# Performance work log

Hardware: AMD Instinct MI355X
Metric: run time of the kernel (lower is better)

Reference implementation:

```python
import jax, jax.numpy as jnp
import numpy as np

TEMPERATURE = 0.1
EPS = 1e-12  # torch F.normalize eps


def _l2_normalize(x):
    n = jnp.linalg.norm(x, axis=1, keepdims=True)
    return x / jnp.maximum(n, EPS)


def setup_inputs() -> dict:
    key = jax.random.key(0)
    k1, k2, k3 = jax.random.split(key, 3)
    B, D = 2048, 2048
    return {
        "emb_i": jax.random.normal(k1, (B, D), dtype=jnp.float32),
        "emb_j": jax.random.normal(k2, (B, D), dtype=jnp.float32),
        "emb_k": jax.random.normal(k3, (B, D), dtype=jnp.float32),
    }


def reference(emb_i, emb_j, emb_k):
    Bi, Bj, Bk = emb_i.shape[0], emb_j.shape[0], emb_k.shape[0]
    size = Bi + Bj + Bk
    Bij = Bi + Bj

    z = jnp.concatenate([
        _l2_normalize(emb_i), _l2_normalize(emb_j), _l2_normalize(emb_k)
    ], axis=0)  # [size, D]

    # cosine similarity of normalized rows == dot product
    sim = z @ z.T                      # [size, size]
    e = jnp.exp(sim / TEMPERATURE)     # [size, size]
    diag = jnp.diagonal(e)             # exp(1/T) on the diagonal

    # denominator per row i: sum over all a != i of exp(sim[i,a]/T)
    denom = e.sum(axis=1) - diag       # [size]

    # rows 0..Bij-1: numerator sums over columns 0..Bij-1, excluding j == i
    num1 = e[:Bij, :Bij].sum(axis=1) - diag[:Bij]
    # rows Bij..size-1: numerator sums over columns Bij..size-1, excluding j == i
    num2 = e[Bij:, Bij:].sum(axis=1) - diag[Bij:]

    loss1 = -jnp.log((num1 / (Bij - 1)) / denom[:Bij])
    loss2 = -jnp.log((num2 / (Bk - 1)) / denom[Bij:])
    return (loss1.sum() + loss2.sum()) / size
```

## Files before the change

kernel.cpp:

```cpp
#include <hip/hip_runtime.h>
#include <hip/hip_bf16.h>

#define SIZE 6144
#define DDIM 2048
#define BHALF 2048
#define BIJ 4096
#define NT 48

typedef __attribute__((ext_vector_type(4))) float f32x4;
typedef __attribute__((ext_vector_type(4))) int i32x4;
typedef __attribute__((ext_vector_type(8))) int i32x8;

__device__ __forceinline__ float block_reduce_sum(float v, float* red) {
    #pragma unroll
    for (int off = 32; off; off >>= 1) v += __shfl_xor(v, off, 64);
    int lane = threadIdx.x & 63, wid = threadIdx.x >> 6;
    if (lane == 0) red[wid] = v;
    __syncthreads();
    float t = red[0] + red[1] + red[2] + red[3];
    __syncthreads();
    return t;
}

__global__ __launch_bounds__(256) void normalize_kernel(
    const float* __restrict__ ei, const float* __restrict__ ej,
    const float* __restrict__ ek,
    unsigned char* __restrict__ zb4, float* __restrict__ dii,
    float* __restrict__ S)
{
    __shared__ float red[4];
    int r = blockIdx.x;
    if (r < 48) S[r * 256 + threadIdx.x] = 0.f;
    const float* src = (r < BHALF)   ? (ei + (size_t)r * DDIM)
                     : (r < 2*BHALF) ? (ej + (size_t)(r - BHALF) * DDIM)
                                     : (ek + (size_t)(r - 2*BHALF) * DDIM);
    int t = threadIdx.x;
    float4 v0 = ((const float4*)src)[t*2];
    float4 v1 = ((const float4*)src)[t*2 + 1];
    float ss = v0.x*v0.x + v0.y*v0.y + v0.z*v0.z + v0.w*v0.w
             + v1.x*v1.x + v1.y*v1.y + v1.z*v1.z + v1.w*v1.w;
    float tot = block_reduce_sum(ss, red);
    float scale = 64.0f / fmaxf(sqrtf(tot), 1e-12f);

    float xs[8] = {v0.x, v0.y, v0.z, v0.w, v1.x, v1.y, v1.z, v1.w};
    unsigned int pk = 0;
    float d = 0.f;
    #pragma unroll
    for (int jj = 0; jj < 8; ++jj) {
        float xv = xs[jj] * scale;
        float ax = fabsf(xv);
        unsigned int m = ax < 0.25f ? 0u : ax < 0.75f ? 1u : ax < 1.25f ? 2u
                       : ax < 1.75f ? 3u : ax < 2.5f  ? 4u : ax < 3.5f  ? 5u
                       : ax < 5.0f  ? 6u : 7u;
        float dec    = ax < 0.25f ? 0.f : ax < 0.75f ? 0.5f : ax < 1.25f ? 1.f
                     : ax < 1.75f ? 1.5f : ax < 2.5f ? 2.f : ax < 3.5f ? 3.f
                     : ax < 5.0f  ? 4.f : 6.f;
        d += dec * dec;
        unsigned int c = m | (xv < 0.f ? 8u : 0u);
        pk |= c << (4 * jj);
    }
    ((unsigned int*)zb4)[(size_t)r * 256 + t] = pk;
    float dtot = block_reduce_sum(d, red);
    if (t == 0) dii[r] = dtot * (1.0f / 4096.0f);
}

__global__ __launch_bounds__(256) void simexp_kernel(
    const unsigned char* __restrict__ zb4, float* __restrict__ S)
{
    __shared__ unsigned char As[2][8192];
    __shared__ unsigned char Bs[2][8192];

    const int x  = blockIdx.x & 7;
    const int j  = blockIdx.x >> 3;
    const int pi = j / 49;
    const int jj = j % 49;
    const int p  = 3 * x + pi;
    int rt, ct;
    if (jj < 48 - p) { rt = p;      ct = p + jj; }
    else             { rt = 47 - p; ct = rt + (jj - (48 - p)); }

    const int tid  = threadIdx.x;
    const int lane = tid & 63;
    const int w    = tid >> 6;
    const int wr   = w >> 1, wc = w & 1;
    const int rowA0 = rt * 128, colB0 = ct * 128;

    const int rowc = lane >> 2;
    const int csw  = (((lane & 3) ^ ((rowc >> 1) & 3))) * 16;

    const int lr = lane & 15;
    const int l4 = lane >> 4;
    const int rsl = ((l4 ^ ((lr >> 1) & 3))) * 16;

    f32x4 acc[4][4] = {};

#define STAGE(buf, kw) do {                                                  \
    _Pragma("unroll")                                                        \
    for (int g2 = 0; g2 < 2; ++g2) {                                         \
        const int g = w * 2 + g2;                                            \
        const unsigned char* ga = zb4                                        \
            + (size_t)(rowA0 + g*16 + rowc) * 1024 + (kw)*64 + csw;          \
        __builtin_amdgcn_global_load_lds(                                    \
            (const __attribute__((address_space(1))) void*)ga,               \
            (__attribute__((address_space(3))) void*)&As[buf][g * 1024],     \
            16, 0, 0);                                                       \
        const unsigned char* gb = zb4                                        \
            + (size_t)(colB0 + g*16 + rowc) * 1024 + (kw)*64 + csw;          \
        __builtin_amdgcn_global_load_lds(                                    \
            (const __attribute__((address_space(1))) void*)gb,               \
            (__attribute__((address_space(3))) void*)&Bs[buf][g * 1024],     \
            16, 0, 0);                                                       \
    }                                                                        \
} while (0)

    STAGE(0, 0);
    __syncthreads();

    for (int t = 0; t < 16; ++t) {
        const int cur = t & 1;
        if (t < 15) STAGE(cur ^ 1, t + 1);

        i32x8 a8[4];
        #pragma unroll
        for (int mi = 0; mi < 4; ++mi) {
            i32x4 tv = *(const i32x4*)&As[cur][(wr*4 + mi)*1024 + lr*64 + rsl];
            a8[mi] = __builtin_shufflevector(tv, tv, 0, 1, 2, 3, -1, -1, -1, -1);
        }
        __builtin_amdgcn_s_setprio(1);
        #pragma unroll
        for (int ni = 0; ni < 4; ++ni) {
            i32x4 tv = *(const i32x4*)&Bs[cur][(wc*4 + ni)*1024 + lr*64 + rsl];
            i32x8 b8 = __builtin_shufflevector(tv, tv, 0, 1, 2, 3, -1, -1, -1, -1);
            #pragma unroll
            for (int mi = 0; mi < 4; ++mi)
                acc[mi][ni] = __builtin_amdgcn_mfma_scale_f32_16x16x128_f8f6f4(
                    a8[mi], b8, acc[mi][ni], 4, 4,
                    0, 0x79797979, 0, 0x79797979);
        }
        __builtin_amdgcn_s_setprio(0);

        if (t < 15) __syncthreads();
    }

    #pragma unroll
    for (int mi = 0; mi < 4; ++mi)
        #pragma unroll
        for (int ni = 0; ni < 4; ++ni)
            #pragma unroll
            for (int q = 0; q < 4; ++q)
                acc[mi][ni][q] = __expf(10.0f * acc[mi][ni][q]);

    {
        float rs[4][4];
        #pragma unroll
        for (int mi = 0; mi < 4; ++mi)
            #pragma unroll
            for (int q = 0; q < 4; ++q) {
                float s = 0.f;
                #pragma unroll
                for (int ni = 0; ni < 4; ++ni) s += acc[mi][ni][q];
                rs[mi][q] = s;
            }
        #pragma unroll
        for (int off = 1; off < 16; off <<= 1)
            #pragma unroll
            for (int mi = 0; mi < 4; ++mi)
                #pragma unroll
                for (int q = 0; q < 4; ++q)
                    rs[mi][q] += __shfl_xor(rs[mi][q], off, 64);

        if ((lane & 15) == 0) {
            float* St = S + ((ct < BIJ / 128) ? 0 : SIZE);
            int rq = l4 * 4;
            #pragma unroll
            for (int mi = 0; mi < 4; ++mi)
                #pragma unroll
                for (int q = 0; q < 4; ++q)
                    atomicAdd(&St[rowA0 + wr*64 + mi*16 + rq + q], rs[mi][q]);
        }
    }

    if (rt != ct) {
        float cs[4];
        #pragma unroll
        for (int ni = 0; ni < 4; ++ni) {
            float s = 0.f;
            #pragma unroll
            for (int mi = 0; mi < 4; ++mi)
                #pragma unroll
                for (int q = 0; q < 4; ++q) s += acc[mi][ni][q];
            cs[ni] = s;
        }
        #pragma unroll
        for (int off = 16; off < 64; off <<= 1)
            #pragma unroll
            for (int ni = 0; ni < 4; ++ni)
                cs[ni] += __shfl_xor(cs[ni], off, 64);

        if (lane < 16) {
            float* St = S + ((rt < BIJ / 128) ? 0 : SIZE);
            #pragma unroll
            for (int ni = 0; ni < 4; ++ni)
                atomicAdd(&St[colB0 + wc*64 + ni*16 + lane], cs[ni]);
        }
    }
}

__global__ __launch_bounds__(256) void loss_kernel(
    const float* __restrict__ S, const float* __restrict__ dii,
    float* __restrict__ out)
{
    __shared__ float red[4];
    float local = 0.f;
    const float c1 = logf((float)(BIJ - 1));
    const float c2 = logf((float)(BHALF - 1));
    for (int r = threadIdx.x; r < SIZE; r += 256) {
        float s1 = S[r], s2 = S[SIZE + r];
        float eii = __expf(10.0f * dii[r]);
        float denom = s1 + s2 - eii;
        float num, c;
        if (r < BIJ) { num = s1 - eii; c = c1; }
        else         { num = s2 - eii; c = c2; }
        local += logf(denom) - logf(num) + c;
    }
    float tot = block_reduce_sum(local, red);
    if (threadIdx.x == 0) out[0] = tot / (float)SIZE;
}

extern "C" void kernel_launch(void* const* d_in, const int* in_sizes, int n_in,
                              void* d_out, int out_size, void* d_ws, size_t ws_size,
                              hipStream_t stream) {
    const float* ei = (const float*)d_in[0];
    const float* ej = (const float*)d_in[1];
    const float* ek = (const float*)d_in[2];
    float* out = (float*)d_out;

    char* ws = (char*)d_ws;
    unsigned char* zb4 = (unsigned char*)ws;
    float* dii = (float*)(ws + 6291456);
    float* S   = (float*)(ws + 6291456 + 24576);

    normalize_kernel<<<dim3(SIZE), dim3(256), 0, stream>>>(ei, ej, ek, zb4, dii, S);
    simexp_kernel<<<dim3(NT * (NT + 1) / 2), dim3(256), 0, stream>>>(zb4, S);
    loss_kernel<<<dim3(1), dim3(256), 0, stream>>>(S, dii, out);
}
```

Before: 78.06 us.

## Split A/B tile staging with fine-grained vmcnt waits and cheaper quantization

The GEMM main loop now issues the A and B tile loads separately, each guarded by its own `s_waitcnt vmcnt` and `s_barrier`. The full `__syncthreads` at the end of each iteration is gone, so the next tile's loads overlap more closely with the current LDS reads and MFMAs. The FP4 e2m1 quantization in the normalize kernel uses a bit-manipulation rounding helper instead of a long chain of compares. The loss kernel merges two logs into one fast `__logf` of the ratio. The hand-written waitcnt assumptions make the schedule fragile, and the fast log and ratio change the rounding slightly.

```diff
diff --git a/kernel.cpp b/kernel.cpp
--- a/kernel.cpp
+++ b/kernel.cpp
@@ -20,6 +20,19 @@
     float t = red[0] + red[1] + red[2] + red[3];
     __syncthreads();
     return t;
+}
+
+__device__ __forceinline__ void quant_e2m1(float xv, unsigned int& code, float& dec) {
+    float ax = fabsf(xv);
+    float y  = fminf(fmaxf(ax, 1.0f), 6.0f);
+    unsigned int u = (__float_as_uint(y) + 0x00200000u) & 0xFFC00000u;
+    float dh = __uint_as_float(u);
+    unsigned int m  = (u >> 22) & 1u;
+    unsigned int e  = ((u >> 23) & 0xFFu) - 127u;
+    unsigned int ch = ((e + 1u) << 1) | m;
+    bool lo = ax < 0.75f, z = ax < 0.25f;
+    dec  = lo ? (z ? 0.f : 0.5f) : dh;
+    code = (lo ? (z ? 0u : 1u) : ch) | (xv < 0.f ? 8u : 0u);
 }
 
 __global__ __launch_bounds__(256) void normalize_kernel(
@@ -47,16 +60,9 @@
     float d = 0.f;
     #pragma unroll
     for (int jj = 0; jj < 8; ++jj) {
-        float xv = xs[jj] * scale;
-        float ax = fabsf(xv);
-        unsigned int m = ax < 0.25f ? 0u : ax < 0.75f ? 1u : ax < 1.25f ? 2u
-                       : ax < 1.75f ? 3u : ax < 2.5f  ? 4u : ax < 3.5f  ? 5u
-                       : ax < 5.0f  ? 6u : 7u;
-        float dec    = ax < 0.25f ? 0.f : ax < 0.75f ? 0.5f : ax < 1.25f ? 1.f
-                     : ax < 1.75f ? 1.5f : ax < 2.5f ? 2.f : ax < 3.5f ? 3.f
-                     : ax < 5.0f  ? 4.f : 6.f;
+        unsigned int c; float dec;
+        quant_e2m1(xs[jj] * scale, c, dec);
         d += dec * dec;
-        unsigned int c = m | (xv < 0.f ? 8u : 0u);
         pk |= c << (4 * jj);
     }
     ((unsigned int*)zb4)[(size_t)r * 256 + t] = pk;
@@ -94,7 +100,7 @@
 
     f32x4 acc[4][4] = {};
 
-#define STAGE(buf, kw) do {                                                  \
+#define STAGE_A(buf, kw) do {                                                \
     _Pragma("unroll")                                                        \
     for (int g2 = 0; g2 < 2; ++g2) {                                         \
         const int g = w * 2 + g2;                                            \
@@ -104,6 +110,13 @@
             (const __attribute__((address_space(1))) void*)ga,               \
             (__attribute__((address_space(3))) void*)&As[buf][g * 1024],     \
             16, 0, 0);                                                       \
+    }                                                                        \
+} while (0)
+
+#define STAGE_B(buf, kw) do {                                                \
+    _Pragma("unroll")                                                        \
+    for (int g2 = 0; g2 < 2; ++g2) {                                         \
+        const int g = w * 2 + g2;                                            \
         const unsigned char* gb = zb4                                        \
             + (size_t)(colB0 + g*16 + rowc) * 1024 + (kw)*64 + csw;          \
         __builtin_amdgcn_global_load_lds(                                    \
@@ -113,19 +126,26 @@
     }                                                                        \
 } while (0)
 
-    STAGE(0, 0);
-    __syncthreads();
+    STAGE_A(0, 0);
+    STAGE_B(0, 0);
 
     for (int t = 0; t < 16; ++t) {
-        const int cur = t & 1;
-        if (t < 15) STAGE(cur ^ 1, t + 1);
-
+        const int cur = t & 1, nxt = cur ^ 1;
+
+        asm volatile("s_waitcnt vmcnt(2)" ::: "memory");
+        asm volatile("s_barrier" ::: "memory");
+        if (t < 15) STAGE_A(nxt, t + 1);
         i32x8 a8[4];
         #pragma unroll
         for (int mi = 0; mi < 4; ++mi) {
             i32x4 tv = *(const i32x4*)&As[cur][(wr*4 + mi)*1024 + lr*64 + rsl];
             a8[mi] = __builtin_shufflevector(tv, tv, 0, 1, 2, 3, -1, -1, -1, -1);
         }
+
+        if (t < 15) { asm volatile("s_waitcnt vmcnt(2)" ::: "memory"); }
+        else        { asm volatile("s_waitcnt vmcnt(0)" ::: "memory"); }
+        asm volatile("s_barrier" ::: "memory");
+        if (t < 15) STAGE_B(nxt, t + 1);
         __builtin_amdgcn_s_setprio(1);
         #pragma unroll
         for (int ni = 0; ni < 4; ++ni) {
@@ -138,8 +158,6 @@
                     0, 0x79797979, 0, 0x79797979);
         }
         __builtin_amdgcn_s_setprio(0);
-
-        if (t < 15) __syncthreads();
     }
 
     #pragma unroll
@@ -221,7 +239,7 @@
         float num, c;
         if (r < BIJ) { num = s1 - eii; c = c1; }
         else         { num = s2 - eii; c = c2; }
-        local += logf(denom) - logf(num) + c;
+        local += __logf(denom / num) + c;
     }
     float tot = block_reduce_sum(local, red);
     if (threadIdx.x == 0) out[0] = tot / (float)SIZE;
```

Result: faster. 70.98 us (-9.1%).
